# Optimization experiments

Hardware: AMD Instinct MI355X
Metric: run time of the kernel (lower is better)

## Reference

```python
import jax, jax.numpy as jnp
import numpy as np

B, C_IN, L = 64, 64, 16384
KS = [1, 3, 5, 7, 9, 11, 13, 15]
OUTC = {1: 1}
for _k in KS[1:]:
    OUTC[_k] = 5


def _conv1d(x, w, b, pad):
    # x: [B, C_in, L], w: [C_out, C_in, K], 'same' padding, stride 1
    y = jax.lax.conv_general_dilated(
        x, w,
        window_strides=(1,),
        padding=[(pad, pad)],
        dimension_numbers=('NCH', 'OIH', 'NCH'),
    )
    return y + b[None, :, None]


def setup_inputs() -> dict:
    key = jax.random.key(0)
    keys = jax.random.split(key, 1 + 2 * len(KS))
    inp = {'x': jax.random.normal(keys[0], (B, C_IN, L), dtype=jnp.float32)}
    scale = 0.05
    for i, k in enumerate(KS):
        oc = OUTC[k]
        inp[f'w{k}'] = jax.random.normal(keys[1 + 2 * i], (oc, C_IN, k), dtype=jnp.float32) * scale
        inp[f'b{k}'] = jax.random.normal(keys[2 + 2 * i], (oc,), dtype=jnp.float32) * scale
    return inp


def reference(x, w1, b1, w3, b3, w5, b5, w7, b7, w9, b9, w11, b11, w13, b13, w15, b15):
    ws = [w1, w3, w5, w7, w9, w11, w13, w15]
    bs = [b1, b3, b5, b7, b9, b11, b13, b15]
    outs = [_conv1d(x, w, b, (k - 1) // 2) for k, w, b in zip(KS, ws, bs)]
    return jnp.concatenate(outs, axis=1)  # [B, 36, L]
```

## Files before the change

kernel.cpp:

```cpp
#include <hip/hip_runtime.h>

typedef __bf16 bf16x8 __attribute__((ext_vector_type(8)));
typedef float f32x4 __attribute__((ext_vector_type(4)));
typedef unsigned short u16x8 __attribute__((ext_vector_type(8)));
typedef unsigned short u16x4 __attribute__((ext_vector_type(4)));

#define L_LEN 16384
#define TILE 256
#define ROWS 270
#define XSTR 72
#define WBT_K 960
#define NOC 48

__device__ __forceinline__ unsigned short f2bf(float f) {
  unsigned u = __builtin_bit_cast(unsigned, f);
  u += 0x7fffu + ((u >> 16) & 1u);
  return (unsigned short)(u >> 16);
}

__device__ __forceinline__ void ocmap(int oc, int& gi, int& lo, int& ks) {
  if (oc == 0)       { gi = 0; lo = 0;       ks = 1;  }
  else if (oc <= 5)  { gi = 1; lo = oc - 1;  ks = 3;  }
  else if (oc <= 10) { gi = 2; lo = oc - 6;  ks = 5;  }
  else if (oc <= 15) { gi = 3; lo = oc - 11; ks = 7;  }
  else if (oc <= 20) { gi = 4; lo = oc - 16; ks = 9;  }
  else if (oc <= 25) { gi = 5; lo = oc - 21; ks = 11; }
  else if (oc <= 31) { gi = -1; lo = 0;      ks = 0;  }
  else if (oc <= 36) { gi = 6; lo = oc - 32; ks = 13; }
  else if (oc <= 41) { gi = 7; lo = oc - 37; ks = 15; }
  else               { gi = -1; lo = 0;      ks = 0;  }
}

__global__ void prep_kernel(const float* w1, const float* b1, const float* w3, const float* b3,
                            const float* w5, const float* b5, const float* w7, const float* b7,
                            const float* w9, const float* b9, const float* w11, const float* b11,
                            const float* w13, const float* b13, const float* w15, const float* b15,
                            unsigned short* wbt, float* bias) {
  const float* ws[8] = {w1, w3, w5, w7, w9, w11, w13, w15};
  const float* bs[8] = {b1, b3, b5, b7, b9, b11, b13, b15};
  int gid = blockIdx.x * 256 + threadIdx.x;
  if (gid < NOC * WBT_K) {
    int oc = gid / WBT_K;
    int kk = gid - oc * WBT_K;
    int t = kk >> 6;
    int c = kk & 63;
    int gi, lo, ks;
    ocmap(oc, gi, lo, ks);
    float v = 0.f;
    if (gi >= 0) {
      int pad = (ks - 1) >> 1;
      int dk = t - 7 + pad;
      if (dk >= 0 && dk < ks) v = ws[gi][(lo * 64 + c) * ks + dk];
    }
    wbt[gid] = f2bf(v);
  }
  if (gid < NOC) {
    int gi, lo, ks;
    ocmap(gid, gi, lo, ks);
    bias[gid] = (gi >= 0) ? bs[gi][lo] : 0.f;
  }
}

template <bool N0, bool N1>
__device__ __forceinline__ void kseg(int ks0, int ks1, const unsigned short* xT, int abase,
                                     const unsigned short* w0, const unsigned short* w1p,
                                     const unsigned short* w2p,
                                     f32x4 (&acc0)[4], f32x4 (&acc1)[4], f32x4 (&acc2)[4]) {
  for (int ksx = ks0; ksx < ks1; ++ksx) {
    const int t = ksx >> 1;
    const int coff = (ksx & 1) * 32;
    bf16x8 a[4];
#pragma unroll
    for (int i = 0; i < 4; ++i) {
      u16x8 raw = *(const u16x8*)(&xT[abase + (i * 16 + t) * XSTR + coff]);
      a[i] = __builtin_bit_cast(bf16x8, raw);
    }
    if (N0) {
      bf16x8 bf = __builtin_bit_cast(bf16x8, *(const u16x8*)(w0 + ksx * 32));
#pragma unroll
      for (int i = 0; i < 4; ++i)
        acc0[i] = __builtin_amdgcn_mfma_f32_16x16x32_bf16(a[i], bf, acc0[i], 0, 0, 0);
    }
    if (N1) {
      bf16x8 bf = __builtin_bit_cast(bf16x8, *(const u16x8*)(w1p + ksx * 32));
#pragma unroll
      for (int i = 0; i < 4; ++i)
        acc1[i] = __builtin_amdgcn_mfma_f32_16x16x32_bf16(a[i], bf, acc1[i], 0, 0, 0);
    }
    {
      bf16x8 bf = __builtin_bit_cast(bf16x8, *(const u16x8*)(w2p + ksx * 32));
#pragma unroll
      for (int i = 0; i < 4; ++i)
        acc2[i] = __builtin_amdgcn_mfma_f32_16x16x32_bf16(a[i], bf, acc2[i], 0, 0, 0);
    }
  }
}

__global__ __launch_bounds__(256, 3)
void Inception1d_62680752718395_kernel(const float* __restrict__ x,
                                       const unsigned short* __restrict__ wbt,
                                       const float* __restrict__ bias,
                                       float* __restrict__ out) {
  __shared__ unsigned short xT[ROWS * XSTR];
  __shared__ unsigned short buf[16 * 272];

  const int tid = threadIdx.x;
  const int bid = blockIdx.x;
  const int tile = bid & 63;
  const int b = bid >> 6;
  const int l0 = tile * TILE;
  const float* xb = x + (size_t)b * 64 * L_LEN;

  for (int cb = 0; cb < 4; ++cb) {
    for (int task = tid; task < 16 * 68; task += 256) {
      int cc = task / 68, ch = task - cc * 68;
      const float* xrow = xb + (size_t)(cb * 16 + cc) * L_LEN;
      int l = l0 - 8 + ch * 4;
      float v[4];
      if (l >= 0 && l + 4 <= L_LEN) {
        f32x4 vv = *(const f32x4*)(xrow + l);
#pragma unroll
        for (int e = 0; e < 4; ++e) v[e] = vv[e];
      } else {
#pragma unroll
        for (int e = 0; e < 4; ++e) {
          int le = l + e;
          v[e] = (le >= 0 && le < L_LEN) ? xrow[le] : 0.f;
        }
      }
      u16x4 p;
#pragma unroll
      for (int e = 0; e < 4; ++e) p[e] = f2bf(v[e]);
      *(u16x4*)(&buf[cc * 272 + ch * 4]) = p;
    }
    __syncthreads();
    for (int task = tid; task < 540; task += 256) {
      int oct = task / 270, r = task - oct * 270;
      u16x8 vv;
#pragma unroll
      for (int j = 0; j < 8; ++j) vv[j] = buf[(oct * 8 + j) * 272 + (r + 1)];
      *(u16x8*)(&xT[r * XSTR + cb * 16 + oct * 8]) = vv;
    }
    __syncthreads();
  }

  const int lane = tid & 63;
  const int wave = tid >> 6;
  const int n15 = lane & 15;
  const int quad = lane >> 4;

  f32x4 acc0[4], acc1[4], acc2[4];
#pragma unroll
  for (int i = 0; i < 4; ++i) {
    acc0[i] = (f32x4){0.f, 0.f, 0.f, 0.f};
    acc1[i] = (f32x4){0.f, 0.f, 0.f, 0.f};
    acc2[i] = (f32x4){0.f, 0.f, 0.f, 0.f};
  }

  const int abase = (wave * 64 + n15) * XSTR + quad * 8;
  const unsigned short* w0p = wbt + (0 + n15) * WBT_K + quad * 8;
  const unsigned short* w1p = wbt + (16 + n15) * WBT_K + quad * 8;
  const unsigned short* w2p = wbt + (32 + n15) * WBT_K + quad * 8;

  kseg<false, false>(0, 4, xT, abase, w0p, w1p, w2p, acc0, acc1, acc2);
  kseg<false, true >(4, 8, xT, abase, w0p, w1p, w2p, acc0, acc1, acc2);
  kseg<true,  true >(8, 22, xT, abase, w0p, w1p, w2p, acc0, acc1, acc2);
  kseg<false, true >(22, 26, xT, abase, w0p, w1p, w2p, acc0, acc1, acc2);
  kseg<false, false>(26, 30, xT, abase, w0p, w1p, w2p, acc0, acc1, acc2);

  const float bs0 = bias[n15];
  const float bs1 = bias[16 + n15];
  const float bs2 = bias[32 + n15];
  const f32x4 bv0 = {bs0, bs0, bs0, bs0};
  const f32x4 bv1 = {bs1, bs1, bs1, bs1};
  const f32x4 bv2 = {bs2, bs2, bs2, bs2};
  const size_t outb = (size_t)b * 36 * L_LEN;
  const int lbase = l0 + wave * 64 + quad * 4;
#pragma unroll
  for (int i = 0; i < 4; ++i) {
    const int lo_ = lbase + i * 16;
    *(f32x4*)(&out[outb + (size_t)n15 * L_LEN + lo_]) = acc0[i] + bv0;
    if (n15 < 10) {
      *(f32x4*)(&out[outb + (size_t)(16 + n15) * L_LEN + lo_]) = acc1[i] + bv1;
      *(f32x4*)(&out[outb + (size_t)(26 + n15) * L_LEN + lo_]) = acc2[i] + bv2;
    }
  }
}

extern "C" void kernel_launch(void* const* d_in, const int* in_sizes, int n_in,
                              void* d_out, int out_size, void* d_ws, size_t ws_size,
                              hipStream_t stream) {
  const float* x = (const float*)d_in[0];
  const float* w[8];
  const float* bb[8];
  for (int i = 0; i < 8; ++i) {
    w[i] = (const float*)d_in[1 + 2 * i];
    bb[i] = (const float*)d_in[2 + 2 * i];
  }
  unsigned short* wbt = (unsigned short*)d_ws;
  float* bias = (float*)((char*)d_ws + NOC * WBT_K * 2);

  prep_kernel<<<(NOC * WBT_K + 255) / 256, 256, 0, stream>>>(
      w[0], bb[0], w[1], bb[1], w[2], bb[2], w[3], bb[3],
      w[4], bb[4], w[5], bb[5], w[6], bb[6], w[7], bb[7], wbt, bias);

  Inception1d_62680752718395_kernel<<<64 * (L_LEN / TILE), 256, 0, stream>>>(
      x, wbt, bias, (float*)d_out);
}
```

Before: 571.5 us.

## Stage input directly into transposed LDS and software-pipeline the MFMA loop

```diff
diff --git a/kernel.cpp b/kernel.cpp
--- a/kernel.cpp
+++ b/kernel.cpp
@@ -3,7 +3,6 @@
 typedef __bf16 bf16x8 __attribute__((ext_vector_type(8)));
 typedef float f32x4 __attribute__((ext_vector_type(4)));
 typedef unsigned short u16x8 __attribute__((ext_vector_type(8)));
-typedef unsigned short u16x4 __attribute__((ext_vector_type(4)));
 
 #define L_LEN 16384
 #define TILE 256
@@ -17,6 +16,9 @@
   u += 0x7fffu + ((u >> 16) & 1u);
   return (unsigned short)(u >> 16);
 }
+
+__device__ __forceinline__ bool act0(int s) { return s >= 8 && s < 22; }
+__device__ __forceinline__ bool act1(int s) { return s >= 4 && s < 26; }
 
 __device__ __forceinline__ void ocmap(int oc, int& gi, int& lo, int& ks) {
   if (oc == 0)       { gi = 0; lo = 0;       ks = 1;  }
@@ -61,48 +63,12 @@
   }
 }
 
-template <bool N0, bool N1>
-__device__ __forceinline__ void kseg(int ks0, int ks1, const unsigned short* xT, int abase,
-                                     const unsigned short* w0, const unsigned short* w1p,
-                                     const unsigned short* w2p,
-                                     f32x4 (&acc0)[4], f32x4 (&acc1)[4], f32x4 (&acc2)[4]) {
-  for (int ksx = ks0; ksx < ks1; ++ksx) {
-    const int t = ksx >> 1;
-    const int coff = (ksx & 1) * 32;
-    bf16x8 a[4];
-#pragma unroll
-    for (int i = 0; i < 4; ++i) {
-      u16x8 raw = *(const u16x8*)(&xT[abase + (i * 16 + t) * XSTR + coff]);
-      a[i] = __builtin_bit_cast(bf16x8, raw);
-    }
-    if (N0) {
-      bf16x8 bf = __builtin_bit_cast(bf16x8, *(const u16x8*)(w0 + ksx * 32));
-#pragma unroll
-      for (int i = 0; i < 4; ++i)
-        acc0[i] = __builtin_amdgcn_mfma_f32_16x16x32_bf16(a[i], bf, acc0[i], 0, 0, 0);
-    }
-    if (N1) {
-      bf16x8 bf = __builtin_bit_cast(bf16x8, *(const u16x8*)(w1p + ksx * 32));
-#pragma unroll
-      for (int i = 0; i < 4; ++i)
-        acc1[i] = __builtin_amdgcn_mfma_f32_16x16x32_bf16(a[i], bf, acc1[i], 0, 0, 0);
-    }
-    {
-      bf16x8 bf = __builtin_bit_cast(bf16x8, *(const u16x8*)(w2p + ksx * 32));
-#pragma unroll
-      for (int i = 0; i < 4; ++i)
-        acc2[i] = __builtin_amdgcn_mfma_f32_16x16x32_bf16(a[i], bf, acc2[i], 0, 0, 0);
-    }
-  }
-}
-
-__global__ __launch_bounds__(256, 3)
+__global__ __launch_bounds__(256, 4)
 void Inception1d_62680752718395_kernel(const float* __restrict__ x,
                                        const unsigned short* __restrict__ wbt,
                                        const float* __restrict__ bias,
                                        float* __restrict__ out) {
   __shared__ unsigned short xT[ROWS * XSTR];
-  __shared__ unsigned short buf[16 * 272];
 
   const int tid = threadIdx.x;
   const int bid = blockIdx.x;
@@ -111,38 +77,32 @@
   const int l0 = tile * TILE;
   const float* xb = x + (size_t)b * 64 * L_LEN;
 
-  for (int cb = 0; cb < 4; ++cb) {
-    for (int task = tid; task < 16 * 68; task += 256) {
-      int cc = task / 68, ch = task - cc * 68;
-      const float* xrow = xb + (size_t)(cb * 16 + cc) * L_LEN;
-      int l = l0 - 8 + ch * 4;
-      float v[4];
-      if (l >= 0 && l + 4 <= L_LEN) {
-        f32x4 vv = *(const f32x4*)(xrow + l);
-#pragma unroll
-        for (int e = 0; e < 4; ++e) v[e] = vv[e];
-      } else {
-#pragma unroll
-        for (int e = 0; e < 4; ++e) {
-          int le = l + e;
-          v[e] = (le >= 0 && le < L_LEN) ? xrow[le] : 0.f;
-        }
+#pragma unroll
+  for (int it = 0; it < 17; ++it) {
+    int task = tid + it * 256;
+    int j = task >> 6;
+    int c = task & 63;
+    const float* xrow = xb + (size_t)c * L_LEN;
+    int l = l0 - 8 + j * 4;
+    float v[4];
+    if (l >= 0 && l + 4 <= L_LEN) {
+      f32x4 vv = *(const f32x4*)(xrow + l);
+#pragma unroll
+      for (int e = 0; e < 4; ++e) v[e] = vv[e];
+    } else {
+#pragma unroll
+      for (int e = 0; e < 4; ++e) {
+        int le = l + e;
+        v[e] = (le >= 0 && le < L_LEN) ? xrow[le] : 0.f;
       }
-      u16x4 p;
-#pragma unroll
-      for (int e = 0; e < 4; ++e) p[e] = f2bf(v[e]);
-      *(u16x4*)(&buf[cc * 272 + ch * 4]) = p;
-    }
-    __syncthreads();
-    for (int task = tid; task < 540; task += 256) {
-      int oct = task / 270, r = task - oct * 270;
-      u16x8 vv;
-#pragma unroll
-      for (int j = 0; j < 8; ++j) vv[j] = buf[(oct * 8 + j) * 272 + (r + 1)];
-      *(u16x8*)(&xT[r * XSTR + cb * 16 + oct * 8]) = vv;
-    }
-    __syncthreads();
-  }
+    }
+#pragma unroll
+    for (int e = 0; e < 4; ++e) {
+      int r = j * 4 + e - 1;
+      if (r >= 0 && r < ROWS) xT[r * XSTR + c] = f2bf(v[e]);
+    }
+  }
+  __syncthreads();
 
   const int lane = tid & 63;
   const int wave = tid >> 6;
@@ -162,11 +122,51 @@
   const unsigned short* w1p = wbt + (16 + n15) * WBT_K + quad * 8;
   const unsigned short* w2p = wbt + (32 + n15) * WBT_K + quad * 8;
 
-  kseg<false, false>(0, 4, xT, abase, w0p, w1p, w2p, acc0, acc1, acc2);
-  kseg<false, true >(4, 8, xT, abase, w0p, w1p, w2p, acc0, acc1, acc2);
-  kseg<true,  true >(8, 22, xT, abase, w0p, w1p, w2p, acc0, acc1, acc2);
-  kseg<false, true >(22, 26, xT, abase, w0p, w1p, w2p, acc0, acc1, acc2);
-  kseg<false, false>(26, 30, xT, abase, w0p, w1p, w2p, acc0, acc1, acc2);
+  bf16x8 aC[4];
+  bf16x8 w0C = {}, w1C = {}, w2C = {};
+  {
+    const int t = 0, coff = 0;
+#pragma unroll
+    for (int i = 0; i < 4; ++i)
+      aC[i] = __builtin_bit_cast(bf16x8, *(const u16x8*)(&xT[abase + (i * 16 + t) * XSTR + coff]));
+    w2C = __builtin_bit_cast(bf16x8, *(const u16x8*)(w2p + 0));
+  }
+
+#pragma unroll
+  for (int s = 0; s < 30; ++s) {
+    bf16x8 aN[4];
+    bf16x8 w0N = {}, w1N = {}, w2N = {};
+    if (s + 1 < 30) {
+      const int sn = s + 1;
+      const int t = sn >> 1;
+      const int coff = (sn & 1) * 32;
+#pragma unroll
+      for (int i = 0; i < 4; ++i)
+        aN[i] = __builtin_bit_cast(bf16x8, *(const u16x8*)(&xT[abase + (i * 16 + t) * XSTR + coff]));
+      if (act0(sn)) w0N = __builtin_bit_cast(bf16x8, *(const u16x8*)(w0p + sn * 32));
+      if (act1(sn)) w1N = __builtin_bit_cast(bf16x8, *(const u16x8*)(w1p + sn * 32));
+      w2N = __builtin_bit_cast(bf16x8, *(const u16x8*)(w2p + sn * 32));
+    } else {
+#pragma unroll
+      for (int i = 0; i < 4; ++i) aN[i] = aC[i];
+    }
+    if (act0(s)) {
+#pragma unroll
+      for (int i = 0; i < 4; ++i)
+        acc0[i] = __builtin_amdgcn_mfma_f32_16x16x32_bf16(aC[i], w0C, acc0[i], 0, 0, 0);
+    }
+    if (act1(s)) {
+#pragma unroll
+      for (int i = 0; i < 4; ++i)
+        acc1[i] = __builtin_amdgcn_mfma_f32_16x16x32_bf16(aC[i], w1C, acc1[i], 0, 0, 0);
+    }
+#pragma unroll
+    for (int i = 0; i < 4; ++i)
+      acc2[i] = __builtin_amdgcn_mfma_f32_16x16x32_bf16(aC[i], w2C, acc2[i], 0, 0, 0);
+#pragma unroll
+    for (int i = 0; i < 4; ++i) aC[i] = aN[i];
+    w0C = w0N; w1C = w1N; w2C = w2N;
+  }
 
   const float bs0 = bias[n15];
   const float bs1 = bias[16 + n15];
```

Measured after the change: 553.9 us. 3.1% less time.
